# Performance work log

Hardware: AMD Instinct MI355X
Metric: run time of the kernel (lower is better)

## Reference

```python
import jax, jax.numpy as jnp
import numpy as np

B, S, H = 2, 2048, 4096
NH, NKV, HD = 32, 8, 128
ROPE_THETA = 10000.0


def _rope_cos_sin():
    inv_freq = 1.0 / (ROPE_THETA ** (jnp.arange(0, HD, 2, dtype=jnp.float32) / HD))  # [HD/2]
    pos = jnp.arange(S, dtype=jnp.float32)
    freqs = pos[:, None] * inv_freq[None, :]            # [S, HD/2]
    emb = jnp.concatenate([freqs, freqs], axis=-1)      # [S, HD]
    cos = jnp.broadcast_to(jnp.cos(emb)[None], (B, S, HD))
    sin = jnp.broadcast_to(jnp.sin(emb)[None], (B, S, HD))
    return cos, sin


def setup_inputs() -> dict:
    key = jax.random.key(0)
    k0, k1, k2, k3, k4 = jax.random.split(key, 5)
    std = 0.02
    hidden_states = jax.random.normal(k0, (B, S, H), dtype=jnp.float32)
    wq = jax.random.normal(k1, (H, NH * HD), dtype=jnp.float32) * std
    wk = jax.random.normal(k2, (H, NKV * HD), dtype=jnp.float32) * std
    wv = jax.random.normal(k3, (H, NKV * HD), dtype=jnp.float32) * std
    wo = jax.random.normal(k4, (NH * HD, H), dtype=jnp.float32) * std
    cos, sin = _rope_cos_sin()
    return {"hidden_states": hidden_states, "cos": cos, "sin": sin,
            "wq": wq, "wk": wk, "wv": wv, "wo": wo}


def _rotate_half(x):
    x1, x2 = jnp.split(x, 2, axis=-1)
    return jnp.concatenate([-x2, x1], axis=-1)


def reference(hidden_states, cos, sin, wq, wk, wv, wo):
    scale = HD ** -0.5
    # QKV projections -> [B, n_heads, S, HD]
    q = (hidden_states @ wq).reshape(B, S, NH, HD).transpose(0, 2, 1, 3)
    k = (hidden_states @ wk).reshape(B, S, NKV, HD).transpose(0, 2, 1, 3)
    v = (hidden_states @ wv).reshape(B, S, NKV, HD).transpose(0, 2, 1, 3)
    # RoPE: cos/sin [B,S,HD] -> broadcast over heads (unsqueeze_dim=1)
    c = cos[:, None, :, :]
    s = sin[:, None, :, :]
    q = q * c + _rotate_half(q) * s
    k = k * c + _rotate_half(k) * s
    # GQA: repeat_interleave kv heads to match query heads
    n_rep = NH // NKV
    k = jnp.repeat(k, n_rep, axis=1)  # [B, NH, S, HD]
    v = jnp.repeat(v, n_rep, axis=1)
    # causal attention
    scores = jnp.einsum('bhqd,bhkd->bhqk', q, k) * scale  # [B,NH,S,S]
    causal = jnp.tril(jnp.ones((S, S), dtype=bool))
    scores = jnp.where(causal[None, None], scores, jnp.finfo(scores.dtype).min)
    probs = jax.nn.softmax(scores, axis=-1)
    attn = jnp.einsum('bhqk,bhkd->bhqd', probs, v)        # [B,NH,S,HD]
    attn = attn.transpose(0, 2, 1, 3).reshape(B, S, NH * HD)
    return attn @ wo
```

## Files before the change

### kernel.cpp

```cpp
#include <hip/hip_runtime.h>

#define B_ 2
#define S_ 2048
#define H_ 4096
#define NH_ 32
#define NKV_ 8
#define HD_ 128
#define QLD 6144

typedef __bf16 bf16;
typedef __bf16 bf16x8 __attribute__((ext_vector_type(8)));
typedef float floatx4 __attribute__((ext_vector_type(4)));
typedef float floatx16 __attribute__((ext_vector_type(16)));
typedef unsigned int u32;

static __device__ __forceinline__ floatx4 fzero4() {
    floatx4 v; v[0] = 0.f; v[1] = 0.f; v[2] = 0.f; v[3] = 0.f; return v;
}

static __device__ __forceinline__ void gload16(const bf16* g, bf16* l) {
    __builtin_amdgcn_global_load_lds((const __attribute__((address_space(1))) u32*)g,
                                     (__attribute__((address_space(3))) u32*)l,
                                     16, 0, 0);
}

__global__ void conv_f32_bf16(const float* __restrict__ in, bf16* __restrict__ out) {
    const long long N = (long long)4096 * 4096;
    long long i = ((long long)blockIdx.x * 256 + threadIdx.x) * 8;
    const long long stride = (long long)gridDim.x * 256 * 8;
    for (; i < N; i += stride) {
        float4 a = *(const float4*)(in + i);
        float4 b = *(const float4*)(in + i + 4);
        bf16x8 h;
        h[0] = (bf16)a.x; h[1] = (bf16)a.y; h[2] = (bf16)a.z; h[3] = (bf16)a.w;
        h[4] = (bf16)b.x; h[5] = (bf16)b.y; h[6] = (bf16)b.z; h[7] = (bf16)b.w;
        *(bf16x8*)(out + i) = h;
    }
}

template <typename TC>
__global__ __launch_bounds__(512) void gemm256(const bf16* __restrict__ A,
                                               const bf16* __restrict__ Bt0,
                                               const bf16* __restrict__ Bt1,
                                               int nsplit,
                                               TC* __restrict__ C,
                                               int lda, int ldC, int col0) {
    __shared__ __align__(16) bf16 lds[2][2][2][8192];

    const int tid  = threadIdx.x;
    const int wid  = tid >> 6;
    const int lane = tid & 63;
    const int quad = lane >> 4;
    const int l16  = lane & 15;
    const int wr   = wid >> 2;
    const int wc   = wid & 3;

    const u32 nbx  = gridDim.x;
    const u32 flat = blockIdx.y * nbx + blockIdx.x;
    const u32 cpx  = (nbx * gridDim.y) >> 3;
    const u32 swz  = (flat & 7) * cpx + (flat >> 3);
    const int m0   = (int)(swz / nbx) * 256;
    const int n0t  = (int)(swz % nbx) * 256;

    const bf16* Bt = (n0t < nsplit) ? Bt0 + (size_t)n0t * 4096
                                    : Bt1 + (size_t)(n0t - nsplit) * 4096;

    floatx4 acc[8][4];
#pragma unroll
    for (int i = 0; i < 8; i++)
#pragma unroll
        for (int j = 0; j < 4; j++) acc[i][j] = fzero4();

    auto stageChunk = [&](int s, int k0, int c) {
        const int op   = c >> 2;
        const int half = (c >> 1) & 1;
        const int r    = (c & 1) * 64 + (tid >> 3);
        const int gs   = tid & 7;
        const int glog = gs ^ (r & 7);
        const int G    = (c & 1) * 512 + tid;
        const bf16* src = op
            ? Bt + (size_t)(half * 128 + r) * 4096 + k0 + glog * 8
            : A + (size_t)(m0 + half * 128 + r) * lda + k0 + glog * 8;
        gload16(src, &lds[s][op][half][(size_t)G * 8]);
    };

    const int NT = 4096 / 64;
#pragma unroll
    for (int c = 0; c < 8; c++) stageChunk(0, 0, c);
#pragma unroll
    for (int c = 0; c < 8; c++) stageChunk(1, 64, c);

    for (int g = 0; g < NT; ++g) {
        const int s = g & 1;
        if (g >= 1 && g + 1 < NT) {
            const int kn = (g + 1) * 64;
#pragma unroll
            for (int c = 0; c < 8; c++) stageChunk((g + 1) & 1, kn, c);
        }
        if (g + 1 < NT) asm volatile("s_waitcnt vmcnt(8)" ::: "memory");
        else            asm volatile("s_waitcnt vmcnt(0)" ::: "memory");
        __builtin_amdgcn_sched_barrier(0);
        __builtin_amdgcn_s_barrier();

#pragma unroll
        for (int p = 0; p < 4; p++) {
            const int qm = p >> 1, qn = p & 1;
            bf16x8 af[4][2], bfr[2][2];
#pragma unroll
            for (int i = 0; i < 4; i++) {
                const int r = (qm * 4 + i) * 16 + l16;
#pragma unroll
                for (int ks = 0; ks < 2; ks++)
                    af[i][ks] = *(const bf16x8*)&lds[s][0][wr]
                        [(size_t)r * 64 + ((ks * 4 + quad) ^ (r & 7)) * 8];
            }
#pragma unroll
            for (int j = 0; j < 2; j++) {
                const int rb = (wc & 1) * 64 + (qn * 2 + j) * 16 + l16;
#pragma unroll
                for (int ks = 0; ks < 2; ks++)
                    bfr[j][ks] = *(const bf16x8*)&lds[s][1][wc >> 1]
                        [(size_t)rb * 64 + ((ks * 4 + quad) ^ (rb & 7)) * 8];
            }
            __builtin_amdgcn_s_barrier();
            __builtin_amdgcn_s_setprio(1);
#pragma unroll
            for (int i = 0; i < 4; i++)
#pragma unroll
                for (int j = 0; j < 2; j++)
#pragma unroll
                    for (int ks = 0; ks < 2; ks++)
                        acc[qm * 4 + i][qn * 2 + j] =
                            __builtin_amdgcn_mfma_f32_16x16x32_bf16(
                                af[i][ks], bfr[j][ks],
                                acc[qm * 4 + i][qn * 2 + j], 0, 0, 0);
            __builtin_amdgcn_s_setprio(0);
            __builtin_amdgcn_s_barrier();
        }
    }

#pragma unroll
    for (int fa = 0; fa < 8; fa++) {
#pragma unroll
        for (int rr = 0; rr < 4; rr++) {
            const int row = m0 + wr * 128 + fa * 16 + quad * 4 + rr;
#pragma unroll
            for (int fb = 0; fb < 4; fb++) {
                const int col = col0 + n0t + wc * 64 + fb * 16 + l16;
                C[(size_t)row * ldC + col] = (TC)acc[fa][fb][rr];
            }
        }
    }
}

template <typename TI, typename TO>
__global__ void transpose_b(const TI* __restrict__ in, TO* __restrict__ out,
                            long long irs, long long ors,
                            int zdiv, long long zs1, long long zs2,
                            long long ozs) {
    __shared__ TI t[32][33];
    const int z = blockIdx.z;
    const TI* ip = in + (long long)(z / zdiv) * zs1 + (long long)(z % zdiv) * zs2;
    TO* op = out + (long long)z * ozs;
    const int r0 = blockIdx.y * 32, c0 = blockIdx.x * 32;
    const int tx = threadIdx.x, ty = threadIdx.y;
#pragma unroll
    for (int i = 0; i < 4; i++)
        t[ty + i * 8][tx] = ip[(long long)(r0 + ty + i * 8) * irs + c0 + tx];
    __syncthreads();
#pragma unroll
    for (int i = 0; i < 4; i++)
        op[(long long)(c0 + ty + i * 8) * ors + r0 + tx] = (TO)t[tx][ty + i * 8];
}

__global__ void rope_q(bf16* __restrict__ q, const float* __restrict__ cosb,
                       const float* __restrict__ sinb) {
    const float QSC = 0.08838834764831845f;
    size_t idx = (size_t)blockIdx.x * 256 + threadIdx.x;
    int dp = idx & 63;
    size_t t = idx >> 6;
    int h = (int)(t % NH_);
    size_t bs = t / NH_;
    size_t base = bs * QLD + (size_t)h * HD_;
    float x1 = (float)q[base + dp];
    float x2 = (float)q[base + dp + 64];
    float c1 = cosb[bs * HD_ + dp];
    float s1 = sinb[bs * HD_ + dp];
    float c2 = cosb[bs * HD_ + dp + 64];
    float s2 = sinb[bs * HD_ + dp + 64];
    q[base + dp]      = (bf16)((x1 * c1 - x2 * s1) * QSC);
    q[base + dp + 64] = (bf16)((x2 * c2 + x1 * s2) * QSC);
}

__global__ void repack_k_rope(const bf16* __restrict__ qkv, bf16* __restrict__ kout,
                              const float* __restrict__ cosb,
                              const float* __restrict__ sinb) {
    size_t idx = (size_t)blockIdx.x * 256 + threadIdx.x;
    int dp = idx & 63;
    size_t t = idx >> 6;
    int kv = (int)(t % NKV_);
    size_t bs = t / NKV_;
    int b = (int)(bs / S_);
    int s = (int)(bs % S_);
    size_t ibase = bs * QLD + (size_t)(NH_ * HD_) + (size_t)kv * HD_;
    float x1 = (float)qkv[ibase + dp];
    float x2 = (float)qkv[ibase + dp + 64];
    float c1 = cosb[bs * HD_ + dp];
    float s1 = sinb[bs * HD_ + dp];
    float c2 = cosb[bs * HD_ + dp + 64];
    float s2 = sinb[bs * HD_ + dp + 64];
    size_t obase = (((size_t)b * NKV_ + kv) * S_ + s) * HD_;
    kout[obase + dp]      = (bf16)(x1 * c1 - x2 * s1);
    kout[obase + dp + 64] = (bf16)(x2 * c2 + x1 * s2);
}

__global__ __launch_bounds__(256) void flash_fwd(const bf16* __restrict__ Q,
                                                 const bf16* __restrict__ Kp,
                                                 const bf16* __restrict__ Vt,
                                                 bf16* __restrict__ O) {
    __shared__ __align__(16) bf16 smem[32768];

    const int bh = blockIdx.y;
    const int b = bh >> 5, h = bh & 31, kv = h >> 2;
    const int tid = threadIdx.x, w = tid >> 6, lane = tid & 63;
    const int l32 = lane & 31, hlf = lane >> 5;

    const bf16* Kb = Kp + (size_t)(b * NKV_ + kv) * S_ * HD_;
    const bf16* Vb = Vt + (size_t)(b * NKV_ + kv) * (size_t)HD_ * S_;
    const bf16* Qbase = Q + (size_t)b * S_ * QLD + (size_t)h * HD_;
    bf16* Obase = O + (size_t)b * S_ * QLD + (size_t)h * HD_;

    auto stage = [&](int kbase, bf16* KsB, bf16* VsB) {
#pragma unroll
        for (int i = 0; i < 4; i++) {
            int G = i * 256 + tid;
            int r = G >> 4, gp = G & 15;
            int gl = gp ^ (r & 15);
            gload16(Kb + (size_t)(kbase + r) * HD_ + gl * 8, KsB + (size_t)G * 8);
        }
#pragma unroll
        for (int i = 0; i < 4; i++) {
            int G = i * 256 + tid;
            int R = G >> 4, gp = G & 15;
            int g16 = gp ^ (R & 15);
            int d = R * 2 + (g16 >> 3);
            int kg = g16 & 7;
            gload16(Vb + (size_t)d * S_ + kbase + kg * 8, VsB + (size_t)G * 8);
        }
    };

    for (int pass = 0; pass < 2; ++pass) {
        const int qb = pass ? (15 - (int)blockIdx.x) : (int)blockIdx.x;
        const int q0 = qb * 128;
        const int wqmin = q0 + w * 32;
        const int wqmax = wqmin + 31;
        const int qrow = wqmin + l32;

        const bf16* Qr = Qbase + (size_t)qrow * QLD;
        bf16x8 qf[8];
#pragma unroll
        for (int ks = 0; ks < 8; ks++)
            qf[ks] = *(const bf16x8*)(Qr + ks * 16 + hlf * 8);

        floatx16 ot[4];
#pragma unroll
        for (int dt = 0; dt < 4; dt++)
#pragma unroll
            for (int r = 0; r < 16; r++) ot[dt][r] = 0.f;
        float mi = -1e30f, li = 0.f;

        if (pass) __syncthreads();
        stage(0, smem, smem + 8192);
        __syncthreads();

        auto compute = [&](int kbase, const bf16* KsB, const bf16* VsB) {
            if (kbase > wqmax) return;
            floatx16 st[2];
#pragma unroll
            for (int n = 0; n < 2; n++)
#pragma unroll
                for (int r = 0; r < 16; r++) st[n][r] = 0.f;
#pragma unroll
            for (int ks = 0; ks < 8; ks++) {
                int phys = (ks * 2 + hlf) ^ (l32 & 15);
#pragma unroll
                for (int n = 0; n < 2; n++) {
                    bf16x8 kf = *(const bf16x8*)(KsB + (size_t)(n * 32 + l32) * 128 + phys * 8);
                    st[n] = __builtin_amdgcn_mfma_f32_32x32x16_bf16(
                        kf, qf[ks], st[n], 0, 0, 0);
                }
            }
            if (kbase + 63 > wqmin) {
#pragma unroll
                for (int n = 0; n < 2; n++)
#pragma unroll
                    for (int r = 0; r < 16; r++) {
                        int key = kbase + n * 32 + (r & 3) + 8 * (r >> 2) + 4 * hlf;
                        if (key > qrow) st[n][r] = -1e30f;
                    }
            }
            float m = st[0][0];
#pragma unroll
            for (int r = 1; r < 16; r++) m = fmaxf(m, st[0][r]);
#pragma unroll
            for (int r = 0; r < 16; r++) m = fmaxf(m, st[1][r]);
            m = fmaxf(m, __shfl_xor(m, 32));
            if (!__all(m <= mi + 8.f)) {
                float mn = fmaxf(mi, m);
                float al = __expf(mi - mn);
                mi = mn;
                li *= al;
#pragma unroll
                for (int dt = 0; dt < 4; dt++)
#pragma unroll
                    for (int r = 0; r < 16; r++) ot[dt][r] *= al;
            }
            float ls = 0.f;
#pragma unroll
            for (int n = 0; n < 2; n++)
#pragma unroll
                for (int r = 0; r < 16; r++) {
                    float p = __expf(st[n][r] - mi);
                    st[n][r] = p;
                    ls += p;
                }
            ls += __shfl_xor(ls, 32);
            li += ls;

            bf16x8 pb[4];
#pragma unroll
            for (int ks2 = 0; ks2 < 4; ks2++) {
                const int n = ks2 >> 1;
                const int rb = (ks2 & 1) * 8;
                float s0 = hlf ? st[n][rb + 0] : st[n][rb + 4];
                float s1 = hlf ? st[n][rb + 1] : st[n][rb + 5];
                float s2 = hlf ? st[n][rb + 2] : st[n][rb + 6];
                float s3 = hlf ? st[n][rb + 3] : st[n][rb + 7];
                float r0 = __shfl_xor(s0, 32);
                float r1 = __shfl_xor(s1, 32);
                float r2 = __shfl_xor(s2, 32);
                float r3 = __shfl_xor(s3, 32);
                float e0, e1, e2, e3, e4, e5, e6, e7;
                if (hlf == 0) {
                    e0 = st[n][rb + 0]; e1 = st[n][rb + 1];
                    e2 = st[n][rb + 2]; e3 = st[n][rb + 3];
                    e4 = r0; e5 = r1; e6 = r2; e7 = r3;
                } else {
                    e0 = r0; e1 = r1; e2 = r2; e3 = r3;
                    e4 = st[n][rb + 4]; e5 = st[n][rb + 5];
                    e6 = st[n][rb + 6]; e7 = st[n][rb + 7];
                }
                bf16x8 t;
                t[0] = (bf16)e0; t[1] = (bf16)e1; t[2] = (bf16)e2; t[3] = (bf16)e3;
                t[4] = (bf16)e4; t[5] = (bf16)e5; t[6] = (bf16)e6; t[7] = (bf16)e7;
                pb[ks2] = t;
            }

#pragma unroll
            for (int ks2 = 0; ks2 < 4; ks2++) {
#pragma unroll
                for (int dt = 0; dt < 4; dt++) {
                    int d = dt * 32 + l32;
                    int g16 = ((d & 1) * 8 + ks2 * 2 + hlf) ^ ((d >> 1) & 15);
                    bf16x8 vf = *(const bf16x8*)(VsB + (size_t)(d >> 1) * 128 + g16 * 8);
                    ot[dt] = __builtin_amdgcn_mfma_f32_32x32x16_bf16(
                        vf, pb[ks2], ot[dt], 0, 0, 0);
                }
            }
        };

        const int nT = 2 * qb + 2;
        for (int j = 0; j < nT; j += 2) {
            stage((j + 1) * 64, smem + 16384, smem + 24576);
            compute(j * 64, smem, smem + 8192);
            __syncthreads();
            if (j + 2 < nT) stage((j + 2) * 64, smem, smem + 8192);
            compute((j + 1) * 64, smem + 16384, smem + 24576);
            __syncthreads();
        }

        {
            const float inv = 1.f / li;
            bf16* Os = smem + (size_t)w * 32 * 136;
#pragma unroll
            for (int dt = 0; dt < 4; dt++)
#pragma unroll
                for (int r = 0; r < 16; r++) {
                    int d = dt * 32 + (r & 3) + 8 * (r >> 2) + 4 * hlf;
                    Os[l32 * 136 + d] = (bf16)(ot[dt][r] * inv);
                }
        }
        __syncthreads();
        {
#pragma unroll
            for (int i = 0; i < 8; i++) {
                int u = i * 256 + tid;
                int qa = u >> 4, gr = u & 15;
                bf16x8 v = *(const bf16x8*)(smem + (size_t)qa * 136 + gr * 8);
                *(bf16x8*)(Obase + (size_t)(q0 + qa) * QLD + gr * 8) = v;
            }
        }
    }
}

extern "C" void kernel_launch(void* const* d_in, const int* in_sizes, int n_in,
                              void* d_out, int out_size, void* d_ws, size_t ws_size,
                              hipStream_t stream) {
    const float* hs   = (const float*)d_in[0];
    const float* cosb = (const float*)d_in[1];
    const float* sinb = (const float*)d_in[2];
    const float* wq   = (const float*)d_in[3];
    const float* wk   = (const float*)d_in[4];
    const float* wv   = (const float*)d_in[5];
    const float* wo   = (const float*)d_in[6];
    float* out = (float*)d_out;
    (void)in_sizes; (void)n_in; (void)out_size;

    const size_t NEED = (size_t)72 * 1024 * 1024;
    if (ws_size < NEED) return;

    char* ws = (char*)d_ws;
    bf16* qkv = (bf16*)ws;
    bf16* R1  = (bf16*)(ws + (size_t)48 * 1024 * 1024);

    bf16* hsb = (bf16*)d_out;
    bf16* BtHi = (bf16*)((char*)d_out + (size_t)32 * 1024 * 1024);

    dim3 tb(32, 8, 1);

    conv_f32_bf16<<<2048, 256, 0, stream>>>(hs, hsb);

    transpose_b<float, bf16><<<dim3(96, 128, 1), tb, 0, stream>>>(
        wq, R1, 4096, 4096, 1, 0, 0, 0);
    transpose_b<float, bf16><<<dim3(32, 128, 1), tb, 0, stream>>>(
        wq + 3072, BtHi, 4096, 4096, 1, 0, 0, 0);
    transpose_b<float, bf16><<<dim3(32, 128, 1), tb, 0, stream>>>(
        wk, BtHi + (size_t)1024 * 4096, 1024, 4096, 1, 0, 0, 0);
    transpose_b<float, bf16><<<dim3(32, 128, 1), tb, 0, stream>>>(
        wv, BtHi + (size_t)2048 * 4096, 1024, 4096, 1, 0, 0, 0);

    gemm256<bf16><<<dim3(24, 16), 512, 0, stream>>>(
        hsb, R1, BtHi, 3072, qkv, 4096, QLD, 0);

    rope_q<<<(B_ * S_ * NH_ * 64) / 256, 256, 0, stream>>>(qkv, cosb, sinb);
    bf16* Kpk = R1;
    bf16* Vtv = R1 + (size_t)B_ * NKV_ * S_ * HD_;
    repack_k_rope<<<(B_ * S_ * NKV_ * 64) / 256, 256, 0, stream>>>(
        qkv, Kpk, cosb, sinb);
    transpose_b<bf16, bf16><<<dim3(HD_ / 32, S_ / 32, B_ * NKV_), tb, 0, stream>>>(
        qkv + NH_ * HD_ + NKV_ * HD_, Vtv, QLD, S_,
        NKV_, (long long)S_ * QLD, HD_, (long long)HD_ * S_);

    flash_fwd<<<dim3(8, B_ * NH_), 256, 0, stream>>>(qkv, Kpk, Vtv, qkv);

    for (int s = 0; s < 2; s++) {
        transpose_b<float, bf16><<<dim3(64, 128, 1), tb, 0, stream>>>(
            wo + 2048 * s, R1, 4096, 4096, 1, 0, 0, 0);
        gemm256<float><<<dim3(8, 16), 512, 0, stream>>>(
            qkv, R1, R1, 1 << 30, out, QLD, 4096, 2048 * s);
    }
}
```

Before: 975.2 us.

## Split QKV output into separate Q and KV buffers and fuse output GEMM

The QKV GEMM now writes Q and KV into separate buffers with their own strides, so the Q buffer is a compact 4096-wide region. That frees workspace, which lets the whole transposed Wo fit (split across two buffers). The output projection then runs as a single 16x16-tile GEMM instead of two sequential half GEMMs with interleaved transposes. This removes one launch and gives the output GEMM a larger grid, at the cost of extra workspace aliasing that must not overlap live data.

```diff
diff --git a/kernel.cpp b/kernel.cpp
--- a/kernel.cpp
+++ b/kernel.cpp
@@ -6,7 +6,8 @@
 #define NH_ 32
 #define NKV_ 8
 #define HD_ 128
-#define QLD 6144
+#define QST 4096
+#define KVS 2048
 
 typedef __bf16 bf16;
 typedef __bf16 bf16x8 __attribute__((ext_vector_type(8)));
@@ -43,8 +44,10 @@
                                                const bf16* __restrict__ Bt0,
                                                const bf16* __restrict__ Bt1,
                                                int nsplit,
-                                               TC* __restrict__ C,
-                                               int lda, int ldC, int col0) {
+                                               TC* __restrict__ C0,
+                                               TC* __restrict__ C1,
+                                               int csplit,
+                                               int lda, int ldC0, int ldC1) {
     __shared__ __align__(16) bf16 lds[2][2][2][8192];
 
     const int tid  = threadIdx.x;
@@ -139,6 +142,9 @@
         }
     }
 
+    TC* Cb; int ldC, cb0;
+    if (n0t < csplit) { Cb = C0; ldC = ldC0; cb0 = n0t; }
+    else              { Cb = C1; ldC = ldC1; cb0 = n0t - csplit; }
 #pragma unroll
     for (int fa = 0; fa < 8; fa++) {
 #pragma unroll
@@ -146,8 +152,8 @@
             const int row = m0 + wr * 128 + fa * 16 + quad * 4 + rr;
 #pragma unroll
             for (int fb = 0; fb < 4; fb++) {
-                const int col = col0 + n0t + wc * 64 + fb * 16 + l16;
-                C[(size_t)row * ldC + col] = (TC)acc[fa][fb][rr];
+                const int col = cb0 + wc * 64 + fb * 16 + l16;
+                Cb[(size_t)row * ldC + col] = (TC)acc[fa][fb][rr];
             }
         }
     }
@@ -181,7 +187,7 @@
     size_t t = idx >> 6;
     int h = (int)(t % NH_);
     size_t bs = t / NH_;
-    size_t base = bs * QLD + (size_t)h * HD_;
+    size_t base = bs * QST + (size_t)h * HD_;
     float x1 = (float)q[base + dp];
     float x2 = (float)q[base + dp + 64];
     float c1 = cosb[bs * HD_ + dp];
@@ -192,7 +198,7 @@
     q[base + dp + 64] = (bf16)((x2 * c2 + x1 * s2) * QSC);
 }
 
-__global__ void repack_k_rope(const bf16* __restrict__ qkv, bf16* __restrict__ kout,
+__global__ void repack_k_rope(const bf16* __restrict__ kvb, bf16* __restrict__ kout,
                               const float* __restrict__ cosb,
                               const float* __restrict__ sinb) {
     size_t idx = (size_t)blockIdx.x * 256 + threadIdx.x;
@@ -202,9 +208,9 @@
     size_t bs = t / NKV_;
     int b = (int)(bs / S_);
     int s = (int)(bs % S_);
-    size_t ibase = bs * QLD + (size_t)(NH_ * HD_) + (size_t)kv * HD_;
-    float x1 = (float)qkv[ibase + dp];
-    float x2 = (float)qkv[ibase + dp + 64];
+    size_t ibase = bs * KVS + (size_t)kv * HD_;
+    float x1 = (float)kvb[ibase + dp];
+    float x2 = (float)kvb[ibase + dp + 64];
     float c1 = cosb[bs * HD_ + dp];
     float s1 = sinb[bs * HD_ + dp];
     float c2 = cosb[bs * HD_ + dp + 64];
@@ -227,8 +233,8 @@
 
     const bf16* Kb = Kp + (size_t)(b * NKV_ + kv) * S_ * HD_;
     const bf16* Vb = Vt + (size_t)(b * NKV_ + kv) * (size_t)HD_ * S_;
-    const bf16* Qbase = Q + (size_t)b * S_ * QLD + (size_t)h * HD_;
-    bf16* Obase = O + (size_t)b * S_ * QLD + (size_t)h * HD_;
+    const bf16* Qbase = Q + (size_t)b * S_ * QST + (size_t)h * HD_;
+    bf16* Obase = O + (size_t)b * S_ * QST + (size_t)h * HD_;
 
     auto stage = [&](int kbase, bf16* KsB, bf16* VsB) {
 #pragma unroll
@@ -256,7 +262,7 @@
         const int wqmax = wqmin + 31;
         const int qrow = wqmin + l32;
 
-        const bf16* Qr = Qbase + (size_t)qrow * QLD;
+        const bf16* Qr = Qbase + (size_t)qrow * QST;
         bf16x8 qf[8];
 #pragma unroll
         for (int ks = 0; ks < 8; ks++)
@@ -397,7 +403,7 @@
                 int u = i * 256 + tid;
                 int qa = u >> 4, gr = u & 15;
                 bf16x8 v = *(const bf16x8*)(smem + (size_t)qa * 136 + gr * 8);
-                *(bf16x8*)(Obase + (size_t)(q0 + qa) * QLD + gr * 8) = v;
+                *(bf16x8*)(Obase + (size_t)(q0 + qa) * QST + gr * 8) = v;
             }
         }
     }
@@ -420,10 +426,12 @@
     if (ws_size < NEED) return;
 
     char* ws = (char*)d_ws;
-    bf16* qkv = (bf16*)ws;
-    bf16* R1  = (bf16*)(ws + (size_t)48 * 1024 * 1024);
-
-    bf16* hsb = (bf16*)d_out;
+    bf16* qbuf = (bf16*)ws;
+    bf16* kvb  = (bf16*)(ws + (size_t)32 * 1024 * 1024);
+    bf16* R1   = (bf16*)(ws + (size_t)48 * 1024 * 1024);
+    bf16* woHi = kvb;
+
+    bf16* hsb  = (bf16*)d_out;
     bf16* BtHi = (bf16*)((char*)d_out + (size_t)32 * 1024 * 1024);
 
     dim3 tb(32, 8, 1);
@@ -440,23 +448,23 @@
         wv, BtHi + (size_t)2048 * 4096, 1024, 4096, 1, 0, 0, 0);
 
     gemm256<bf16><<<dim3(24, 16), 512, 0, stream>>>(
-        hsb, R1, BtHi, 3072, qkv, 4096, QLD, 0);
-
-    rope_q<<<(B_ * S_ * NH_ * 64) / 256, 256, 0, stream>>>(qkv, cosb, sinb);
+        hsb, R1, BtHi, 3072, qbuf, kvb, 4096, 4096, QST, KVS);
+
+    rope_q<<<(B_ * S_ * NH_ * 64) / 256, 256, 0, stream>>>(qbuf, cosb, sinb);
     bf16* Kpk = R1;
     bf16* Vtv = R1 + (size_t)B_ * NKV_ * S_ * HD_;
     repack_k_rope<<<(B_ * S_ * NKV_ * 64) / 256, 256, 0, stream>>>(
-        qkv, Kpk, cosb, sinb);
+        kvb, Kpk, cosb, sinb);
     transpose_b<bf16, bf16><<<dim3(HD_ / 32, S_ / 32, B_ * NKV_), tb, 0, stream>>>(
-        qkv + NH_ * HD_ + NKV_ * HD_, Vtv, QLD, S_,
-        NKV_, (long long)S_ * QLD, HD_, (long long)HD_ * S_);
-
-    flash_fwd<<<dim3(8, B_ * NH_), 256, 0, stream>>>(qkv, Kpk, Vtv, qkv);
-
-    for (int s = 0; s < 2; s++) {
-        transpose_b<float, bf16><<<dim3(64, 128, 1), tb, 0, stream>>>(
-            wo + 2048 * s, R1, 4096, 4096, 1, 0, 0, 0);
-        gemm256<float><<<dim3(8, 16), 512, 0, stream>>>(
-            qkv, R1, R1, 1 << 30, out, QLD, 4096, 2048 * s);
-    }
-}
+        kvb + 1024, Vtv, KVS, S_,
+        NKV_, (long long)S_ * KVS, HD_, (long long)HD_ * S_);
+
+    flash_fwd<<<dim3(8, B_ * NH_), 256, 0, stream>>>(qbuf, Kpk, Vtv, qbuf);
+
+    transpose_b<float, bf16><<<dim3(96, 128, 1), tb, 0, stream>>>(
+        wo, R1, 4096, 4096, 1, 0, 0, 0);
+    transpose_b<float, bf16><<<dim3(32, 128, 1), tb, 0, stream>>>(
+        wo + 3072, woHi, 4096, 4096, 1, 0, 0, 0);
+    gemm256<float><<<dim3(16, 16), 512, 0, stream>>>(
+        qbuf, R1, woHi, 3072, out, out, 1 << 30, QST, 4096, 4096);
+}
```

Measured after the change: 842.1 us. 13.7% less time.
